# Performance work log

Hardware: AMD Instinct MI355X
Metric: run time of the kernel (lower is better)

The kernel has to match this reference:

```python
import jax, jax.numpy as jnp
import numpy as np
from itertools import combinations

NUM_FIELDS = 32
EMB = 64
# static pair index lists for combinations(range(NUM_FIELDS), 2)
_PAIRS = np.array(list(combinations(range(NUM_FIELDS), 2)), dtype=np.int32)  # (496, 2)
I_IDX = jnp.asarray(_PAIRS[:, 0])
J_IDX = jnp.asarray(_PAIRS[:, 1])


def bilinear_each(feats, W):
    # feats: (B, F, E); W: (F-1, E, E) with torch Linear convention y = x @ W[i].T
    # transform fields 0..F-2 with their own weight
    t = jnp.einsum('bfe,foe->bfo', feats[:, :NUM_FIELDS - 1, :], W)  # (B, F-1, E)
    # pair (i, j): t[:, i] * feats[:, j]
    return t[:, I_IDX, :] * feats[:, J_IDX, :]  # (B, P, E)


def se_block(x, se_w1, se_w2):
    # x: (B, F, E)
    Z = jnp.mean(x, axis=-1)                      # (B, F)
    A = jax.nn.relu(Z @ se_w1.T)                  # (B, F//r)
    A = jax.nn.sigmoid(A @ se_w2.T)               # (B, F)
    return x * A[:, :, None]


def setup_inputs() -> dict:
    key = jax.random.key(0)
    ks = jax.random.split(key, 12)
    B, F, E = 1024, NUM_FIELDS, EMB
    P = F * (F - 1) // 2
    d_in = 2 * P * E  # 63488
    h1, h2, nc = 1024, 512, 1
    red = max(1, F // 8)
    s = lambda *sh: 1.0 / np.sqrt(sh[-1])
    inp = {
        'x': jax.random.normal(ks[0], (B, F, E), dtype=jnp.float32),
        'W_bil1': jax.random.normal(ks[1], (F - 1, E, E), jnp.float32) * s(E),
        'W_bil2': jax.random.normal(ks[2], (F - 1, E, E), jnp.float32) * s(E),
        'se_w1': jax.random.normal(ks[3], (red, F), jnp.float32) * s(F),
        'se_w2': jax.random.normal(ks[4], (F, red), jnp.float32) * s(red),
        'fc0_w': jax.random.normal(ks[5], (h1, d_in), jnp.float32) * s(d_in),
        'fc0_b': jnp.zeros((h1,), jnp.float32),
        'fc1_w': jax.random.normal(ks[6], (h2, h1), jnp.float32) * s(h1),
        'fc1_b': jnp.zeros((h2,), jnp.float32),
        'fc2_w': jax.random.normal(ks[7], (nc, h2), jnp.float32) * s(h2),
        'fc2_b': jnp.zeros((nc,), jnp.float32),
    }
    return inp


def reference(x, W_bil1, W_bil2, se_w1, se_w2, fc0_w, fc0_b, fc1_w, fc1_b, fc2_w, fc2_b):
    f1 = bilinear_each(x, W_bil1)                    # (B, P, E)
    f2 = bilinear_each(se_block(x, se_w1, se_w2), W_bil2)  # (B, P, E)
    feat = jnp.concatenate([f1, f2], axis=1).reshape(x.shape[0], -1)  # (B, 2*P*E)
    h = jax.nn.relu(feat @ fc0_w.T + fc0_b)
    h = jax.nn.relu(h @ fc1_w.T + fc1_b)
    y = jax.nn.sigmoid(h @ fc2_w.T + fc2_b)
    return y
```

## Files before the change

### kernel.cpp

```cpp
#include <hip/hip_runtime.h>
#include <hip/hip_bf16.h>
#include <stdint.h>


typedef __attribute__((ext_vector_type(4))) int   int4v;
typedef __attribute__((ext_vector_type(4))) unsigned uint4v;
typedef __attribute__((ext_vector_type(4))) float f32x4;

__device__ __forceinline__ unsigned short f32_bf16(float f) {
  unsigned u = __builtin_bit_cast(unsigned, f);
  u = (u + 0x7fffu + ((u >> 16) & 1u)) >> 16;
  return (unsigned short)u;
}
__device__ __forceinline__ unsigned pk_bf16(float lo, float hi) {
  return (unsigned)f32_bf16(lo) | ((unsigned)f32_bf16(hi) << 16);
}
__device__ __forceinline__ unsigned cvt_pk(float lo, float hi) {
  unsigned r;
  asm("v_cvt_pk_bf16_f32 %0, %1, %2" : "=v"(r) : "v"(lo), "v"(hi));
  return r;
}

__global__ __launch_bounds__(256) void se_kernel(
    const float* __restrict__ x, const float* __restrict__ w1,
    const float* __restrict__ w2, float* __restrict__ scale) {
  __shared__ float Z[32];
  __shared__ float A1[4];
  int b = blockIdx.x;
  int t = threadIdx.x;
  int f = t >> 3, sub = t & 7;
  const float4* xp = (const float4*)(x + (size_t)b * 2048 + f * 64 + sub * 8);
  float4 v0 = xp[0], v1 = xp[1];
  float s = v0.x + v0.y + v0.z + v0.w + v1.x + v1.y + v1.z + v1.w;
  s += __shfl_down(s, 4, 8);
  s += __shfl_down(s, 2, 8);
  s += __shfl_down(s, 1, 8);
  if (sub == 0) Z[f] = s * (1.0f / 64.0f);
  __syncthreads();
  if (t < 4) {
    float a = 0.f;
#pragma unroll
    for (int ff = 0; ff < 32; ++ff) a += Z[ff] * w1[t * 32 + ff];
    A1[t] = fmaxf(a, 0.f);
  }
  __syncthreads();
  if (t < 32) {
    float a = 0.f;
#pragma unroll
    for (int r = 0; r < 4; ++r) a += A1[r] * w2[t * 4 + r];
    scale[b * 32 + t] = 1.f / (1.f + expf(-a));
  }
}

__global__ __launch_bounds__(256) void t_kernel(
    const float* __restrict__ x, const float* __restrict__ W1,
    const float* __restrict__ W2, const float* __restrict__ scale,
    float* __restrict__ t1, float* __restrict__ t2) {
  __shared__ float Wl[64 * 65];
  __shared__ float xs[64 * 65];
  int f = blockIdx.x;
  int b0 = blockIdx.y * 64;
  int which = blockIdx.z;
  const float* W = (which ? W2 : W1) + (size_t)f * 4096;
  float* tout = which ? t2 : t1;
  int t = threadIdx.x;
#pragma unroll
  for (int it = 0; it < 16; ++it) {
    int idx = it * 256 + t;
    int o = idx >> 6, e = idx & 63;
    Wl[o * 65 + e] = W[idx];
  }
#pragma unroll
  for (int it = 0; it < 16; ++it) {
    int idx = it * 256 + t;
    int bl = idx >> 6, e = idx & 63;
    float v = x[(size_t)(b0 + bl) * 2048 + f * 64 + e];
    if (which) v *= scale[(b0 + bl) * 32 + f];
    xs[bl * 65 + e] = v;
  }
  __syncthreads();
  int o = t & 63, g = t >> 6;
  float sum[16];
#pragma unroll
  for (int r = 0; r < 16; ++r) sum[r] = 0.f;
#pragma unroll 4
  for (int e = 0; e < 64; ++e) {
    float wv = Wl[o * 65 + e];
#pragma unroll
    for (int r = 0; r < 16; ++r) sum[r] += xs[(g * 16 + r) * 65 + e] * wv;
  }
#pragma unroll
  for (int r = 0; r < 16; ++r)
    tout[(size_t)(b0 + g * 16 + r) * 1984 + f * 64 + o] = sum[r];
}

__global__ __launch_bounds__(256) void feat_kernel(
    const float* __restrict__ x, const float* __restrict__ t1,
    const float* __restrict__ t2, const float* __restrict__ scale,
    unsigned short* __restrict__ feat) {
  int gid = blockIdx.x * 256 + threadIdx.x;
  int b = gid / 7936;
  int rem = gid - b * 7936;
  int s = rem >> 3;
  int e0 = (rem & 7) * 8;
  int which = (s >= 496) ? 1 : 0;
  int p = s - (which ? 496 : 0);
  int i = (int)((63.0f - sqrtf((float)(3969 - 8 * p))) * 0.5f);
  while ((i * (63 - i)) / 2 > p) --i;
  while (((i + 1) * (62 - i)) / 2 <= p) ++i;
  int j = i + 1 + (p - (i * (63 - i)) / 2);
  const float* tp = (which ? t2 : t1) + (size_t)b * 1984 + i * 64 + e0;
  const float* xp = x + (size_t)b * 2048 + j * 64 + e0;
  float sc = which ? scale[b * 32 + j] : 1.0f;
  float4 ta = *(const float4*)tp, tb = *(const float4*)(tp + 4);
  float4 xa = *(const float4*)xp, xb = *(const float4*)(xp + 4);
  uint4v o;
  o.x = pk_bf16(ta.x * xa.x * sc, ta.y * xa.y * sc);
  o.y = pk_bf16(ta.z * xa.z * sc, ta.w * xa.w * sc);
  o.z = pk_bf16(tb.x * xb.x * sc, tb.y * xb.y * sc);
  o.w = pk_bf16(tb.z * xb.z * sc, tb.w * xb.w * sc);
  *(uint4v*)(feat + (size_t)b * 63488 + s * 64 + e0) = o;
}

__device__ __forceinline__ void mfma_bf16(f32x4& d, int4v a, int4v b) {
  asm volatile("v_mfma_f32_16x16x32_bf16 %0, %1, %2, %0"
               : "+v"(d) : "v"(a), "v"(b));
}

#define FBM 256
#define FBN 256
#define FBK 64

__device__ __forceinline__ void fc0_phase(
    const unsigned short* sAb, const unsigned short* sBb,
    int kk, int wr, int wc, int l15, int l4, f32x4 (&acc)[8][4]) {
  int4v av[8], bv[4];
#pragma unroll
  for (int i = 0; i < 8; ++i) {
    int ar = wr + i * 16 + l15;
    av[i] = *(const int4v*)&sAb[(ar * 8 + ((kk * 4 + l4) ^ (ar & 7))) * 8];
  }
#pragma unroll
  for (int j = 0; j < 4; ++j) {
    int br = wc + j * 16 + l15;
    bv[j] = *(const int4v*)&sBb[(br * 8 + ((kk * 4 + l4) ^ (br & 7))) * 8];
  }
#pragma unroll
  for (int i = 0; i < 8; ++i)
#pragma unroll
    for (int j = 0; j < 4; ++j) mfma_bf16(acc[i][j], av[i], bv[j]);
}

__global__ __launch_bounds__(512, 2) void gemm_fc0(
    const unsigned short* __restrict__ A, const float* __restrict__ Bp,
    float* __restrict__ Cp, int M, int N, int K, int kz) {
  __shared__ unsigned short sA[2][FBM * FBK];
  __shared__ unsigned short sB[2][FBN * FBK];
  int tid = threadIdx.x;
  int lane = tid & 63;
  int wave = tid >> 6;
  int bid = blockIdx.x;
  int m0 = (bid >> 6) << 8;
  int s  = bid & 63;
  int n0 = (s & 3) << 8;
  int z  = s >> 2;
  int wr = (wave >> 2) * 128, wc = (wave & 3) * 64;
  int l15 = lane & 15, l4 = lane >> 4;
  int kbase = z * kz;
  int nt = kz / FBK;

  f32x4 acc[8][4];
#pragma unroll
  for (int i = 0; i < 8; ++i)
#pragma unroll
    for (int j = 0; j < 4; ++j) acc[i][j] = (f32x4){0.f, 0.f, 0.f, 0.f};

  unsigned aOff[4]; int aDst[4];
  unsigned bOff[4]; int bDst[4];
#pragma unroll
  for (int it = 0; it < 4; ++it) {
    int c = it * 512 + tid;
    int r = c >> 3, l = c & 7;
    aOff[it] = (unsigned)(m0 + r) * (unsigned)K + (unsigned)((l ^ (r & 7)) << 3);
    aDst[it] = c * 8;
    bOff[it] = (unsigned)(n0 + r) * (unsigned)K + (unsigned)(l << 3);
    bDst[it] = (r * 8 + (l ^ (r & 7))) * 8;
  }

#define FC0_STAGE_A(buf, kt)                                                   \
  _Pragma("unroll") for (int it = 0; it < 4; ++it) {                           \
    __builtin_amdgcn_global_load_lds(                                          \
        (const __attribute__((address_space(1))) void*)(A + aOff[it] + (kt)),  \
        (__attribute__((address_space(3))) void*)(&sA[buf][aDst[it]]), 16, 0, 0); \
  }
#define FC0_LOAD_B(kt)                                                         \
  _Pragma("unroll") for (int it = 0; it < 4; ++it) {                           \
    const float* gp = Bp + bOff[it] + (kt);                                    \
    bst[2 * it]     = *(const float4*)gp;                                      \
    bst[2 * it + 1] = *(const float4*)(gp + 4);                                \
  }
#define FC0_WRITE_B(buf)                                                       \
  _Pragma("unroll") for (int it = 0; it < 4; ++it) {                           \
    uint4v q;                                                                  \
    q.x = cvt_pk(bst[2 * it].x, bst[2 * it].y);                                \
    q.y = cvt_pk(bst[2 * it].z, bst[2 * it].w);                                \
    q.z = cvt_pk(bst[2 * it + 1].x, bst[2 * it + 1].y);                        \
    q.w = cvt_pk(bst[2 * it + 1].z, bst[2 * it + 1].w);                        \
    *(uint4v*)(&sB[buf][bDst[it]]) = q;                                        \
  }
#define FENCE_VMEM() __builtin_amdgcn_sched_barrier(0x38F)

  float4 bst[8];
  FC0_LOAD_B(kbase)
  FENCE_VMEM();
  FC0_WRITE_B(0)
  FC0_STAGE_A(0, kbase)
  FENCE_VMEM();
  FC0_LOAD_B(kbase + FBK)
  asm volatile("s_waitcnt vmcnt(8) lgkmcnt(0)" ::: "memory");
  __builtin_amdgcn_s_barrier();

  int t = 0;
#pragma unroll 2
  for (; t < nt - 2; ++t) {
    int cur = t & 1, nxt = cur ^ 1;
    FC0_STAGE_A(nxt, kbase + (t + 1) * FBK)
    fc0_phase(sA[cur], sB[cur], 0, wr, wc, l15, l4, acc);
    FENCE_VMEM();
    FC0_WRITE_B(nxt)
    FC0_LOAD_B(kbase + (t + 2) * FBK)
    fc0_phase(sA[cur], sB[cur], 1, wr, wc, l15, l4, acc);
    asm volatile("s_waitcnt vmcnt(8) lgkmcnt(0)" ::: "memory");
    __builtin_amdgcn_s_barrier();
  }
  {
    int cur = t & 1, nxt = cur ^ 1;
    FC0_STAGE_A(nxt, kbase + (t + 1) * FBK)
    fc0_phase(sA[cur], sB[cur], 0, wr, wc, l15, l4, acc);
    FC0_WRITE_B(nxt)
    fc0_phase(sA[cur], sB[cur], 1, wr, wc, l15, l4, acc);
    asm volatile("s_waitcnt vmcnt(0) lgkmcnt(0)" ::: "memory");
    __builtin_amdgcn_s_barrier();
    ++t;
    cur = t & 1;
    fc0_phase(sA[cur], sB[cur], 0, wr, wc, l15, l4, acc);
    fc0_phase(sA[cur], sB[cur], 1, wr, wc, l15, l4, acc);
  }
#undef FC0_STAGE_A
#undef FC0_LOAD_B
#undef FC0_WRITE_B
#undef FENCE_VMEM

  asm volatile("s_nop 7\n\ts_nop 7\n\ts_nop 7" ::: "memory");
  float* cp = Cp + (size_t)z * M * N;
#pragma unroll
  for (int i = 0; i < 8; ++i) {
    int rbase = m0 + wr + i * 16 + l4 * 4;
#pragma unroll
    for (int j = 0; j < 4; ++j) {
      int cc = n0 + wc + j * 16 + l15;
#pragma unroll
      for (int r = 0; r < 4; ++r)
        cp[(size_t)(rbase + r) * N + cc] = acc[i][j][r];
    }
  }
}

#define BM 256
#define BN 128
#define BK 64

__global__ __launch_bounds__(256, 2) void gemm_bt(
    const unsigned short* __restrict__ A, const float* __restrict__ B,
    float* __restrict__ Cp, int M, int N, int K, int kz) {
  __shared__ unsigned short sA[BM * BK];
  __shared__ unsigned short sB[BN * BK];
  int tid = threadIdx.x;
  int lane = tid & 63, wave = tid >> 6;
  int n0 = blockIdx.x * BN, m0 = blockIdx.y * BM;
  int z = blockIdx.z;
  int wr = (wave >> 1) * 128, wc = (wave & 1) * 64;
  int l15 = lane & 15, l4 = lane >> 4;
  f32x4 acc[8][4];
#pragma unroll
  for (int i = 0; i < 8; ++i)
#pragma unroll
    for (int j = 0; j < 4; ++j) acc[i][j] = (f32x4){0.f, 0.f, 0.f, 0.f};

  int kend = z * kz + kz;
  for (int kt = z * kz; kt < kend; kt += BK) {
#pragma unroll
    for (int it = 0; it < 8; ++it) {
      int c = it * 256 + tid;
      int r = c >> 3, p = c & 7;
      int gcol = (p ^ (r & 7)) * 8;
      const unsigned short* gp = A + (size_t)(m0 + r) * K + kt + gcol;
      __builtin_amdgcn_global_load_lds(
          (const __attribute__((address_space(1))) void*)gp,
          (__attribute__((address_space(3))) void*)(&sA[c * 8]), 16, 0, 0);
    }
#pragma unroll
    for (int it = 0; it < 4; ++it) {
      int c = it * 256 + tid;
      int r = c >> 3, l = c & 7;
      const float* gp = B + (size_t)(n0 + r) * K + kt + l * 8;
      float4 f0 = *(const float4*)gp;
      float4 f1 = *(const float4*)(gp + 4);
      uint4v q;
      q.x = pk_bf16(f0.x, f0.y); q.y = pk_bf16(f0.z, f0.w);
      q.z = pk_bf16(f1.x, f1.y); q.w = pk_bf16(f1.z, f1.w);
      int p = l ^ (r & 7);
      *(uint4v*)(&sB[(r * 8 + p) * 8]) = q;
    }
    __syncthreads();
#pragma unroll
    for (int kk = 0; kk < 2; ++kk) {
      int lc = kk * 4 + l4;
      int4v av[8], bv[4];
#pragma unroll
      for (int i = 0; i < 8; ++i) {
        int ar = wr + i * 16 + l15;
        av[i] = *(const int4v*)&sA[(ar * 8 + (lc ^ (ar & 7))) * 8];
      }
#pragma unroll
      for (int j = 0; j < 4; ++j) {
        int br = wc + j * 16 + l15;
        bv[j] = *(const int4v*)&sB[(br * 8 + (lc ^ (br & 7))) * 8];
      }
#pragma unroll
      for (int i = 0; i < 8; ++i)
#pragma unroll
        for (int j = 0; j < 4; ++j) mfma_bf16(acc[i][j], av[i], bv[j]);
    }
    __syncthreads();
  }
  asm volatile("s_nop 7\n\ts_nop 7\n\ts_nop 7" ::: "memory");
  float* cp = Cp + (size_t)z * M * N;
#pragma unroll
  for (int i = 0; i < 8; ++i) {
    int rbase = m0 + wr + i * 16 + l4 * 4;
#pragma unroll
    for (int j = 0; j < 4; ++j) {
      int cc = n0 + wc + j * 16 + l15;
#pragma unroll
      for (int r = 0; r < 4; ++r)
        cp[(size_t)(rbase + r) * N + cc] = acc[i][j][r];
    }
  }
}

__global__ __launch_bounds__(256) void reduce_bias_act(
    const float* __restrict__ parts, const float* __restrict__ bias,
    int MN, int nmask, int nz, unsigned short* __restrict__ out_bf,
    float* __restrict__ out_f) {
  int idx = blockIdx.x * 256 + threadIdx.x;
  if (idx >= MN) return;
  float s = 0.f;
  for (int z = 0; z < nz; ++z) s += parts[(size_t)z * MN + idx];
  s += bias[idx & nmask];
  s = fmaxf(s, 0.f);
  if (out_bf) out_bf[idx] = f32_bf16(s);
  else out_f[idx] = s;
}

__global__ __launch_bounds__(256) void fc2_kernel(
    const float* __restrict__ h2, const float* __restrict__ w,
    const float* __restrict__ b, float* __restrict__ out) {
  int wave = threadIdx.x >> 6, lane = threadIdx.x & 63;
  int row = blockIdx.x * 4 + wave;
  const float4* hp = (const float4*)(h2 + (size_t)row * 512);
  const float4* wp = (const float4*)w;
  int i0 = lane * 2;
  float4 a0 = hp[i0], a1 = hp[i0 + 1];
  float4 w0 = wp[i0], w1 = wp[i0 + 1];
  float s = a0.x * w0.x + a0.y * w0.y + a0.z * w0.z + a0.w * w0.w +
            a1.x * w1.x + a1.y * w1.y + a1.z * w1.z + a1.w * w1.w;
#pragma unroll
  for (int off = 32; off > 0; off >>= 1) s += __shfl_down(s, off);
  if (lane == 0) out[row] = 1.f / (1.f + expf(-(s + b[0])));
}

extern "C" void kernel_launch(void* const* d_in, const int* in_sizes, int n_in,
                              void* d_out, int out_size, void* d_ws, size_t ws_size,
                              hipStream_t stream) {
  const float* x     = (const float*)d_in[0];
  const float* Wb1   = (const float*)d_in[1];
  const float* Wb2   = (const float*)d_in[2];
  const float* se_w1 = (const float*)d_in[3];
  const float* se_w2 = (const float*)d_in[4];
  const float* fc0_w = (const float*)d_in[5];
  const float* fc0_b = (const float*)d_in[6];
  const float* fc1_w = (const float*)d_in[7];
  const float* fc1_b = (const float*)d_in[8];
  const float* fc2_w = (const float*)d_in[9];
  const float* fc2_b = (const float*)d_in[10];
  (void)in_sizes; (void)n_in; (void)out_size; (void)ws_size;

  char* ws = (char*)d_ws;
  float*          scale = (float*)(ws + 0);
  float*          t1    = (float*)(ws + 131072);
  float*          t2    = (float*)(ws + 8257536);
  unsigned short* feat  = (unsigned short*)(ws + 16384000);
  float*          hp    = (float*)(ws + 146407424);
  unsigned short* h1b   = (unsigned short*)(ws + 213516288);
  float*          h2    = (float*)(ws + 215613440);
  float*          out   = (float*)d_out;

  se_kernel<<<1024, 256, 0, stream>>>(x, se_w1, se_w2, scale);
  t_kernel<<<dim3(31, 16, 2), 256, 0, stream>>>(x, Wb1, Wb2, scale, t1, t2);
  feat_kernel<<<31744, 256, 0, stream>>>(x, t1, t2, scale, feat);
  gemm_fc0<<<256, 512, 0, stream>>>(feat, fc0_w, hp, 1024, 1024, 63488, 3968);
  reduce_bias_act<<<4096, 256, 0, stream>>>(hp, fc0_b, 1024 * 1024, 1023, 16, h1b, nullptr);
  gemm_bt<<<dim3(4, 4, 16), 256, 0, stream>>>(h1b, fc1_w, hp, 1024, 512, 1024, 64);
  reduce_bias_act<<<2048, 256, 0, stream>>>(hp, fc1_b, 1024 * 512, 511, 16, nullptr, h2);
  fc2_kernel<<<256, 256, 0, stream>>>(h2, fc2_w, fc2_b, out);
}
```

Baseline: 537.1 us.

## Fuse pairwise feature construction into fc0 GEMM A-tile loading

```diff
diff --git a/kernel.cpp b/kernel.cpp
--- a/kernel.cpp
+++ b/kernel.cpp
@@ -23,9 +23,11 @@
 
 __global__ __launch_bounds__(256) void se_kernel(
     const float* __restrict__ x, const float* __restrict__ w1,
-    const float* __restrict__ w2, float* __restrict__ scale) {
+    const float* __restrict__ w2, float* __restrict__ scale,
+    float* __restrict__ xs2) {
   __shared__ float Z[32];
   __shared__ float A1[4];
+  __shared__ float Sc[32];
   int b = blockIdx.x;
   int t = threadIdx.x;
   int f = t >> 3, sub = t & 7;
@@ -48,8 +50,17 @@
     float a = 0.f;
 #pragma unroll
     for (int r = 0; r < 4; ++r) a += A1[r] * w2[t * 4 + r];
-    scale[b * 32 + t] = 1.f / (1.f + expf(-a));
-  }
+    float sg = 1.f / (1.f + expf(-a));
+    scale[b * 32 + t] = sg;
+    Sc[t] = sg;
+  }
+  __syncthreads();
+  float sc = Sc[f];
+  float4 o0, o1;
+  o0.x = v0.x * sc; o0.y = v0.y * sc; o0.z = v0.z * sc; o0.w = v0.w * sc;
+  o1.x = v1.x * sc; o1.y = v1.y * sc; o1.z = v1.z * sc; o1.w = v1.w * sc;
+  float4* op = (float4*)(xs2 + (size_t)b * 2048 + f * 64 + sub * 8);
+  op[0] = o0; op[1] = o1;
 }
 
 __global__ __launch_bounds__(256) void t_kernel(
@@ -94,34 +105,6 @@
     tout[(size_t)(b0 + g * 16 + r) * 1984 + f * 64 + o] = sum[r];
 }
 
-__global__ __launch_bounds__(256) void feat_kernel(
-    const float* __restrict__ x, const float* __restrict__ t1,
-    const float* __restrict__ t2, const float* __restrict__ scale,
-    unsigned short* __restrict__ feat) {
-  int gid = blockIdx.x * 256 + threadIdx.x;
-  int b = gid / 7936;
-  int rem = gid - b * 7936;
-  int s = rem >> 3;
-  int e0 = (rem & 7) * 8;
-  int which = (s >= 496) ? 1 : 0;
-  int p = s - (which ? 496 : 0);
-  int i = (int)((63.0f - sqrtf((float)(3969 - 8 * p))) * 0.5f);
-  while ((i * (63 - i)) / 2 > p) --i;
-  while (((i + 1) * (62 - i)) / 2 <= p) ++i;
-  int j = i + 1 + (p - (i * (63 - i)) / 2);
-  const float* tp = (which ? t2 : t1) + (size_t)b * 1984 + i * 64 + e0;
-  const float* xp = x + (size_t)b * 2048 + j * 64 + e0;
-  float sc = which ? scale[b * 32 + j] : 1.0f;
-  float4 ta = *(const float4*)tp, tb = *(const float4*)(tp + 4);
-  float4 xa = *(const float4*)xp, xb = *(const float4*)(xp + 4);
-  uint4v o;
-  o.x = pk_bf16(ta.x * xa.x * sc, ta.y * xa.y * sc);
-  o.y = pk_bf16(ta.z * xa.z * sc, ta.w * xa.w * sc);
-  o.z = pk_bf16(tb.x * xb.x * sc, tb.y * xb.y * sc);
-  o.w = pk_bf16(tb.z * xb.z * sc, tb.w * xb.w * sc);
-  *(uint4v*)(feat + (size_t)b * 63488 + s * 64 + e0) = o;
-}
-
 __device__ __forceinline__ void mfma_bf16(f32x4& d, int4v a, int4v b) {
   asm volatile("v_mfma_f32_16x16x32_bf16 %0, %1, %2, %0"
                : "+v"(d) : "v"(a), "v"(b));
@@ -152,21 +135,24 @@
 }
 
 __global__ __launch_bounds__(512, 2) void gemm_fc0(
-    const unsigned short* __restrict__ A, const float* __restrict__ Bp,
-    float* __restrict__ Cp, int M, int N, int K, int kz) {
+    const float* __restrict__ T1, const float* __restrict__ T2,
+    const float* __restrict__ X, const float* __restrict__ XS2,
+    const float* __restrict__ Bp, float* __restrict__ Cp, int kz) {
   __shared__ unsigned short sA[2][FBM * FBK];
   __shared__ unsigned short sB[2][FBN * FBK];
+  const int K = 63488;
   int tid = threadIdx.x;
   int lane = tid & 63;
   int wave = tid >> 6;
   int bid = blockIdx.x;
   int m0 = (bid >> 6) << 8;
-  int s  = bid & 63;
-  int n0 = (s & 3) << 8;
-  int z  = s >> 2;
+  int sb = bid & 63;
+  int n0 = (sb & 3) << 8;
+  int z  = sb >> 2;
   int wr = (wave >> 2) * 128, wc = (wave & 3) * 64;
   int l15 = lane & 15, l4 = lane >> 4;
   int kbase = z * kz;
+  int s0 = kbase >> 6;
   int nt = kz / FBK;
 
   f32x4 acc[8][4];
@@ -175,84 +161,141 @@
 #pragma unroll
     for (int j = 0; j < 4; ++j) acc[i][j] = (f32x4){0.f, 0.f, 0.f, 0.f};
 
-  unsigned aOff[4]; int aDst[4];
-  unsigned bOff[4]; int bDst[4];
+  unsigned rtOff[4], rxOff[4], bOff[4]; int sDst[4];
 #pragma unroll
   for (int it = 0; it < 4; ++it) {
     int c = it * 512 + tid;
     int r = c >> 3, l = c & 7;
-    aOff[it] = (unsigned)(m0 + r) * (unsigned)K + (unsigned)((l ^ (r & 7)) << 3);
-    aDst[it] = c * 8;
-    bOff[it] = (unsigned)(n0 + r) * (unsigned)K + (unsigned)(l << 3);
-    bDst[it] = (r * 8 + (l ^ (r & 7))) * 8;
-  }
-
-#define FC0_STAGE_A(buf, kt)                                                   \
-  _Pragma("unroll") for (int it = 0; it < 4; ++it) {                           \
-    __builtin_amdgcn_global_load_lds(                                          \
-        (const __attribute__((address_space(1))) void*)(A + aOff[it] + (kt)),  \
-        (__attribute__((address_space(3))) void*)(&sA[buf][aDst[it]]), 16, 0, 0); \
-  }
-#define FC0_LOAD_B(kt)                                                         \
+    sDst[it] = (r * 8 + (l ^ (r & 7))) * 8;
+    rtOff[it] = (unsigned)(m0 + r) * 1984u + (unsigned)(l * 8);
+    rxOff[it] = (unsigned)(m0 + r) * 2048u + (unsigned)(l * 8);
+    bOff[it]  = (unsigned)(n0 + r) * (unsigned)K + (unsigned)(l * 8);
+  }
+
+  float4 ast0[8];
+  float4 ast1[8];
+  float4 bst[8];
+  const float* tpc = T1;
+  const float* xpc = X;
+
+  auto set_pair = [&](int s) {
+    int which = (s >= 496);
+    int p = s - (which ? 496 : 0);
+    int i = (int)((63.0f - sqrtf((float)(3969 - 8 * p))) * 0.5f);
+    while ((i * (63 - i)) / 2 > p) --i;
+    while (((i + 1) * (62 - i)) / 2 <= p) ++i;
+    int j = i + 1 + (p - (i * (63 - i)) / 2);
+    tpc = (which ? T2 : T1) + i * 64;
+    xpc = (which ? XS2 : X) + j * 64;
+  };
+
+#define FC0_ALOAD0()                                                           \
+  _Pragma("unroll") for (int it = 0; it < 2; ++it) {                           \
+    ast0[it * 4 + 0] = *(const float4*)(tpc + rtOff[it]);                      \
+    ast0[it * 4 + 1] = *(const float4*)(tpc + rtOff[it] + 4);                  \
+    ast0[it * 4 + 2] = *(const float4*)(xpc + rxOff[it]);                      \
+    ast0[it * 4 + 3] = *(const float4*)(xpc + rxOff[it] + 4);                  \
+  }
+#define FC0_ALOAD1()                                                           \
+  _Pragma("unroll") for (int it = 2; it < 4; ++it) {                           \
+    ast1[(it - 2) * 4 + 0] = *(const float4*)(tpc + rtOff[it]);                \
+    ast1[(it - 2) * 4 + 1] = *(const float4*)(tpc + rtOff[it] + 4);            \
+    ast1[(it - 2) * 4 + 2] = *(const float4*)(xpc + rxOff[it]);                \
+    ast1[(it - 2) * 4 + 3] = *(const float4*)(xpc + rxOff[it] + 4);            \
+  }
+#define FC0_AWRITE0(buf)                                                       \
+  _Pragma("unroll") for (int it = 0; it < 2; ++it) {                           \
+    int q = it * 4;                                                            \
+    uint4v o;                                                                  \
+    o.x = cvt_pk(ast0[q].x * ast0[q + 2].x, ast0[q].y * ast0[q + 2].y);        \
+    o.y = cvt_pk(ast0[q].z * ast0[q + 2].z, ast0[q].w * ast0[q + 2].w);        \
+    o.z = cvt_pk(ast0[q + 1].x * ast0[q + 3].x, ast0[q + 1].y * ast0[q + 3].y);\
+    o.w = cvt_pk(ast0[q + 1].z * ast0[q + 3].z, ast0[q + 1].w * ast0[q + 3].w);\
+    *(uint4v*)(&sA[buf][sDst[it]]) = o;                                        \
+  }
+#define FC0_AWRITE1(buf)                                                       \
+  _Pragma("unroll") for (int it = 2; it < 4; ++it) {                           \
+    int q = (it - 2) * 4;                                                      \
+    uint4v o;                                                                  \
+    o.x = cvt_pk(ast1[q].x * ast1[q + 2].x, ast1[q].y * ast1[q + 2].y);        \
+    o.y = cvt_pk(ast1[q].z * ast1[q + 2].z, ast1[q].w * ast1[q + 2].w);        \
+    o.z = cvt_pk(ast1[q + 1].x * ast1[q + 3].x, ast1[q + 1].y * ast1[q + 3].y);\
+    o.w = cvt_pk(ast1[q + 1].z * ast1[q + 3].z, ast1[q + 1].w * ast1[q + 3].w);\
+    *(uint4v*)(&sA[buf][sDst[it]]) = o;                                        \
+  }
+#define FC0_BLOAD(kt)                                                          \
   _Pragma("unroll") for (int it = 0; it < 4; ++it) {                           \
     const float* gp = Bp + bOff[it] + (kt);                                    \
     bst[2 * it]     = *(const float4*)gp;                                      \
     bst[2 * it + 1] = *(const float4*)(gp + 4);                                \
   }
-#define FC0_WRITE_B(buf)                                                       \
+#define FC0_BWRITE(buf)                                                        \
   _Pragma("unroll") for (int it = 0; it < 4; ++it) {                           \
-    uint4v q;                                                                  \
-    q.x = cvt_pk(bst[2 * it].x, bst[2 * it].y);                                \
-    q.y = cvt_pk(bst[2 * it].z, bst[2 * it].w);                                \
-    q.z = cvt_pk(bst[2 * it + 1].x, bst[2 * it + 1].y);                        \
-    q.w = cvt_pk(bst[2 * it + 1].z, bst[2 * it + 1].w);                        \
-    *(uint4v*)(&sB[buf][bDst[it]]) = q;                                        \
-  }
-#define FENCE_VMEM() __builtin_amdgcn_sched_barrier(0x38F)
-
-  float4 bst[8];
-  FC0_LOAD_B(kbase)
-  FENCE_VMEM();
-  FC0_WRITE_B(0)
-  FC0_STAGE_A(0, kbase)
-  FENCE_VMEM();
-  FC0_LOAD_B(kbase + FBK)
-  asm volatile("s_waitcnt vmcnt(8) lgkmcnt(0)" ::: "memory");
+    uint4v o;                                                                  \
+    o.x = cvt_pk(bst[2 * it].x, bst[2 * it].y);                                \
+    o.y = cvt_pk(bst[2 * it].z, bst[2 * it].w);                                \
+    o.z = cvt_pk(bst[2 * it + 1].x, bst[2 * it + 1].y);                        \
+    o.w = cvt_pk(bst[2 * it + 1].z, bst[2 * it + 1].w);                        \
+    *(uint4v*)(&sB[buf][sDst[it]]) = o;                                        \
+  }
+#define VMW(n) asm volatile("s_waitcnt vmcnt(" #n ")" ::: "memory")
+
+  set_pair(s0);
+  FC0_ALOAD0()
+  VMW(0);
+  FC0_AWRITE0(0)
+  FC0_ALOAD1()
+  VMW(0);
+  FC0_AWRITE1(0)
+  FC0_BLOAD(kbase)
+  VMW(0);
+  FC0_BWRITE(0)
+  FC0_BLOAD(kbase + FBK)
+  asm volatile("s_waitcnt lgkmcnt(0)" ::: "memory");
   __builtin_amdgcn_s_barrier();
 
-  int t = 0;
+#define FC0_TILE(cur, nxt, SNEXT, KT2, DO_B)                                   \
+  {                                                                            \
+    fc0_phase(sA[cur], sB[cur], 0, wr, wc, l15, l4, acc);                      \
+    set_pair(SNEXT);                                                           \
+    FC0_ALOAD0()                                                               \
+    VMW(8);                                                                    \
+    FC0_BWRITE(nxt)                                                            \
+    FC0_ALOAD1()                                                               \
+    VMW(8);                                                                    \
+    FC0_AWRITE0(nxt)                                                           \
+    if (DO_B) { FC0_BLOAD(KT2) VMW(8); } else { VMW(0); }                      \
+    FC0_AWRITE1(nxt)                                                           \
+    fc0_phase(sA[cur], sB[cur], 1, wr, wc, l15, l4, acc);                      \
+    asm volatile("s_waitcnt lgkmcnt(0)" ::: "memory");                         \
+    __builtin_amdgcn_s_barrier();                                              \
+  }
+
 #pragma unroll 2
-  for (; t < nt - 2; ++t) {
+  for (int t = 0; t < nt - 2; ++t) {
     int cur = t & 1, nxt = cur ^ 1;
-    FC0_STAGE_A(nxt, kbase + (t + 1) * FBK)
-    fc0_phase(sA[cur], sB[cur], 0, wr, wc, l15, l4, acc);
-    FENCE_VMEM();
-    FC0_WRITE_B(nxt)
-    FC0_LOAD_B(kbase + (t + 2) * FBK)
-    fc0_phase(sA[cur], sB[cur], 1, wr, wc, l15, l4, acc);
-    asm volatile("s_waitcnt vmcnt(8) lgkmcnt(0)" ::: "memory");
-    __builtin_amdgcn_s_barrier();
+    FC0_TILE(cur, nxt, s0 + t + 1, kbase + (t + 2) * FBK, 1)
   }
   {
-    int cur = t & 1, nxt = cur ^ 1;
-    FC0_STAGE_A(nxt, kbase + (t + 1) * FBK)
-    fc0_phase(sA[cur], sB[cur], 0, wr, wc, l15, l4, acc);
-    FC0_WRITE_B(nxt)
-    fc0_phase(sA[cur], sB[cur], 1, wr, wc, l15, l4, acc);
-    asm volatile("s_waitcnt vmcnt(0) lgkmcnt(0)" ::: "memory");
-    __builtin_amdgcn_s_barrier();
-    ++t;
-    cur = t & 1;
+    int t = nt - 2, cur = t & 1, nxt = cur ^ 1;
+    FC0_TILE(cur, nxt, s0 + t + 1, 0, 0)
+  }
+  {
+    int cur = (nt - 1) & 1;
     fc0_phase(sA[cur], sB[cur], 0, wr, wc, l15, l4, acc);
     fc0_phase(sA[cur], sB[cur], 1, wr, wc, l15, l4, acc);
   }
-#undef FC0_STAGE_A
-#undef FC0_LOAD_B
-#undef FC0_WRITE_B
-#undef FENCE_VMEM
+#undef FC0_TILE
+#undef FC0_ALOAD0
+#undef FC0_ALOAD1
+#undef FC0_AWRITE0
+#undef FC0_AWRITE1
+#undef FC0_BLOAD
+#undef FC0_BWRITE
+#undef VMW
 
   asm volatile("s_nop 7\n\ts_nop 7\n\ts_nop 7" ::: "memory");
-  float* cp = Cp + (size_t)z * M * N;
+  float* cp = Cp + (size_t)z * 1024 * 1024;
 #pragma unroll
   for (int i = 0; i < 8; ++i) {
     int rbase = m0 + wr + i * 16 + l4 * 4;
@@ -261,7 +304,7 @@
       int cc = n0 + wc + j * 16 + l15;
 #pragma unroll
       for (int r = 0; r < 4; ++r)
-        cp[(size_t)(rbase + r) * N + cc] = acc[i][j][r];
+        cp[(size_t)(rbase + r) * 1024 + cc] = acc[i][j][r];
     }
   }
 }
@@ -400,16 +443,15 @@
   float*          scale = (float*)(ws + 0);
   float*          t1    = (float*)(ws + 131072);
   float*          t2    = (float*)(ws + 8257536);
-  unsigned short* feat  = (unsigned short*)(ws + 16384000);
-  float*          hp    = (float*)(ws + 146407424);
-  unsigned short* h1b   = (unsigned short*)(ws + 213516288);
-  float*          h2    = (float*)(ws + 215613440);
+  float*          xs2   = (float*)(ws + 16384000);
+  float*          hp    = (float*)(ws + 24772608);
+  unsigned short* h1b   = (unsigned short*)(ws + 91881472);
+  float*          h2    = (float*)(ws + 93978624);
   float*          out   = (float*)d_out;
 
-  se_kernel<<<1024, 256, 0, stream>>>(x, se_w1, se_w2, scale);
+  se_kernel<<<1024, 256, 0, stream>>>(x, se_w1, se_w2, scale, xs2);
   t_kernel<<<dim3(31, 16, 2), 256, 0, stream>>>(x, Wb1, Wb2, scale, t1, t2);
-  feat_kernel<<<31744, 256, 0, stream>>>(x, t1, t2, scale, feat);
-  gemm_fc0<<<256, 512, 0, stream>>>(feat, fc0_w, hp, 1024, 1024, 63488, 3968);
+  gemm_fc0<<<256, 512, 0, stream>>>(t1, t2, x, xs2, fc0_w, hp, 3968);
   reduce_bias_act<<<4096, 256, 0, stream>>>(hp, fc0_b, 1024 * 1024, 1023, 16, h1b, nullptr);
   gemm_bt<<<dim3(4, 4, 16), 256, 0, stream>>>(h1b, fc1_w, hp, 1024, 512, 1024, 64);
   reduce_bias_act<<<2048, 256, 0, stream>>>(hp, fc1_b, 1024 * 512, 511, 16, nullptr, h2);
```

New measurement: 643.6 us. 1.2x slower.
